# Performance work log

Measured on AMD Instinct MI355X. Metric: run time of the kernel, lower is better.

Reference implementation:

```python
import jax, jax.numpy as jnp
import numpy as np

B, N, E, H = 4, 2048, 1024, 16
Dh = E // H  # 64


def _rope_tables(n, dh, dtype=jnp.float32):
    inv_freq = 1.0 / (10000.0 ** (jnp.arange(0, dh, 2, dtype=jnp.float32) / dh))
    t = jnp.arange(n, dtype=jnp.float32)
    freqs = jnp.outer(t, inv_freq)            # (N, Dh/2)
    emb = jnp.concatenate([freqs, freqs], -1)  # (N, Dh)
    return jnp.cos(emb).astype(dtype), jnp.sin(emb).astype(dtype)


def _rotate_half(x):
    half = x.shape[-1] // 2
    return jnp.concatenate([-x[..., half:], x[..., :half]], axis=-1)


def _apply_rope(x, cos, sin):
    # x: (B, H, N, Dh); cos/sin: (N, Dh)
    return x * cos[None, None] + _rotate_half(x) * sin[None, None]


def setup_inputs() -> dict:
    key = jax.random.key(0)
    ks = jax.random.split(key, 10)
    x = jax.random.normal(ks[0], (B, N, E), dtype=jnp.float32)
    s = 0.02
    wq = jax.random.normal(ks[1], (E, E), jnp.float32) * s
    bq = jnp.zeros((E,), jnp.float32)
    wk = jax.random.normal(ks[2], (E, E), jnp.float32) * s
    bk = jnp.zeros((E,), jnp.float32)
    wv = jax.random.normal(ks[3], (E, E), jnp.float32) * s
    bv = jnp.zeros((E,), jnp.float32)
    wo = jax.random.normal(ks[4], (E, E), jnp.float32) * s
    bo = jnp.zeros((E,), jnp.float32)
    # no padding (all keys valid); flip some entries True to exercise masking if desired
    key_padding_mask = jnp.zeros((B, N), dtype=bool)
    return dict(x=x, wq=wq, bq=bq, wk=wk, bk=bk, wv=wv, bv=bv,
                wo=wo, bo=bo, key_padding_mask=key_padding_mask)


def reference(x, wq, bq, wk, bk, wv, bv, wo, bo, key_padding_mask):
    b, n, e = x.shape

    def proj(w, bvec):
        y = jnp.einsum('bne,fe->bnf', x, w) + bvec  # Linear: x @ W^T + b
        return y.reshape(b, n, H, Dh).transpose(0, 2, 1, 3)  # (B,H,N,Dh)

    Q, K, V = proj(wq, bq), proj(wk, bk), proj(wv, bv)
    cos, sin = _rope_tables(n, Dh, x.dtype)
    Q = _apply_rope(Q, cos, sin)
    K = _apply_rope(K, cos, sin)

    scale = Dh ** -0.5
    attn = jnp.einsum('bhqd,bhkd->bhqk', Q, K) * scale  # (B,H,N,N)
    attn = jnp.where(key_padding_mask[:, None, None, :], -jnp.inf, attn)
    attn = jax.nn.softmax(attn, axis=-1)
    out = jnp.einsum('bhqk,bhkd->bhqd', attn, V)
    out = out.transpose(0, 2, 1, 3).reshape(b, n, e)
    return jnp.einsum('bne,fe->bnf', out, wo) + bo
```

## Files before the change

### kernel.cpp

```cpp
#include <hip/hip_runtime.h>
#include <hip/hip_bf16.h>
#include <stdint.h>

#define B_   4
#define N_   2048
#define E_   1024
#define H_   16
#define DH_  64
#define M_   (B_*N_)
#define KD_  1024

typedef __bf16 bf16x8 __attribute__((ext_vector_type(8)));
typedef float  f32x4  __attribute__((ext_vector_type(4)));
typedef float  f32x16 __attribute__((ext_vector_type(16)));

__device__ __forceinline__ ushort f2bf(float f) {
  union { float f; uint32_t u; } x; x.f = f;
  uint32_t r = x.u + 0x7fffu + ((x.u >> 16) & 1u);
  return (ushort)(r >> 16);
}

__device__ __forceinline__ f32x4 mfma16(bf16x8 a, bf16x8 b, f32x4 c) {
  return __builtin_amdgcn_mfma_f32_16x16x32_bf16(a, b, c, 0, 0, 0);
}
__device__ __forceinline__ f32x16 mfma32(bf16x8 a, bf16x8 b, f32x16 c) {
  return __builtin_amdgcn_mfma_f32_32x32x16_bf16(a, b, c, 0, 0, 0);
}

__device__ __forceinline__ uint32_t cvtpk(float lo, float hi) {
  uint32_t d;
  asm("v_cvt_pk_bf16_f32 %0, %1, %2" : "=v"(d) : "v"(lo), "v"(hi));
  return d;
}

#if __has_builtin(__builtin_amdgcn_exp2f)
#define FEXP2(x) __builtin_amdgcn_exp2f(x)
#else
#define FEXP2(x) exp2f(x)
#endif

__device__ __forceinline__ void gload16(const void* g, void* l) {
  __builtin_amdgcn_global_load_lds(
      (const __attribute__((address_space(1))) uint32_t*)g,
      (__attribute__((address_space(3))) uint32_t*)l, 16, 0, 0);
}

__global__ void prep(const float* __restrict__ x,
                     const float* __restrict__ wq, const float* __restrict__ wk,
                     const float* __restrict__ wv, const float* __restrict__ wo,
                     ushort* __restrict__ xb, ushort* __restrict__ wqkv,
                     ushort* __restrict__ wob,
                     float* __restrict__ ct, float* __restrict__ st)
{
  int bid = blockIdx.x;
  if (bid < 8192) {
    int i = (bid * 256 + threadIdx.x) * 4;
    float4 v = *(const float4*)(x + i);
    ushort4 o; o.x = f2bf(v.x); o.y = f2bf(v.y); o.z = f2bf(v.z); o.w = f2bf(v.w);
    *(ushort4*)(xb + i) = o;
  } else if (bid < 12288) {
    int i = ((bid - 8192) * 256 + threadIdx.x) * 4;
    int which = i >> 20;
    int off = i & 1048575;
    const float* src = which == 0 ? wq : which == 1 ? wk : which == 2 ? wv : wo;
    float4 v = *(const float4*)(src + off);
    ushort4 o; o.x = f2bf(v.x); o.y = f2bf(v.y); o.z = f2bf(v.z); o.w = f2bf(v.w);
    if (which < 3) *(ushort4*)(wqkv + i) = o;
    else           *(ushort4*)(wob + off) = o;
  } else {
    int idx = (bid - 12288) * 256 + threadIdx.x;
    int n = idx >> 5, i = idx & 31;
    double inv = exp(-(double)i * (9.210340371976184 / 32.0));
    float ang = (float)n * (float)inv;
    ct[idx] = cosf(ang);
    st[idx] = sinf(ang);
  }
}

#define GEMM_KLOOP(Aptr, Wptr)                                                 \
  for (int k0 = 0; k0 < KD_; k0 += 64) {                                       \
    _Pragma("unroll")                                                          \
    for (int i = 0; i < 4; ++i) {                                              \
      uint32_t flat = i * 4096 + w * 1024 + lane * 16;                         \
      uint32_t row = flat >> 7, cb = flat & 127;                               \
      uint32_t cbs = cb ^ ((row & 7) << 4);                                    \
      gload16((const char*)(Aptr) + (size_t)(m0 + row) * 2048 + k0 * 2 + cbs,  \
              smA + i * 4096 + w * 1024);                                      \
      gload16((const char*)(Wptr) + (size_t)(n0 + row) * 2048 + k0 * 2 + cbs,  \
              smB + i * 4096 + w * 1024);                                      \
    }                                                                          \
    __syncthreads();                                                           \
    bf16x8 af[4][2], bfr[4][2];                                                \
    _Pragma("unroll")                                                          \
    for (int mf = 0; mf < 4; ++mf)                                             \
      _Pragma("unroll")                                                        \
      for (int kk = 0; kk < 2; ++kk) {                                         \
        int row = wr * 64 + mf * 16 + c;                                       \
        int cb = (kk * 64 + g * 16) ^ ((row & 7) << 4);                        \
        af[mf][kk] = *(const bf16x8*)(smA + row * 128 + cb);                   \
        int rowb = wc * 64 + mf * 16 + c;                                      \
        int cbb = (kk * 64 + g * 16) ^ ((rowb & 7) << 4);                      \
        bfr[mf][kk] = *(const bf16x8*)(smB + rowb * 128 + cbb);                \
      }                                                                        \
    _Pragma("unroll")                                                          \
    for (int kk = 0; kk < 2; ++kk)                                             \
      _Pragma("unroll")                                                        \
      for (int mf = 0; mf < 4; ++mf)                                           \
        _Pragma("unroll")                                                      \
        for (int nf = 0; nf < 4; ++nf)                                         \
          acc[mf][nf] = mfma16(af[mf][kk], bfr[nf][kk], acc[mf][nf]);          \
    __syncthreads();                                                           \
  }

__launch_bounds__(256, 3)
__global__ void gemm_qkv(const ushort* __restrict__ A, const ushort* __restrict__ W,
                         const float* __restrict__ bq, const float* __restrict__ bk,
                         const float* __restrict__ bv,
                         ushort* __restrict__ Qo, ushort* __restrict__ Ko,
                         ushort* __restrict__ Vto,
                         const float* __restrict__ cost, const float* __restrict__ sint)
{
  __shared__ char smem[32768];
  char* smA = smem;
  char* smB = smem + 16384;
  const int tid = threadIdx.x;
  const int lane = tid & 63, w = tid >> 6;
  const int c = lane & 15, g = lane >> 4;
  const int m0 = blockIdx.x * 128, n0 = blockIdx.y * 128;
  const int wr = w >> 1, wc = w & 1;

  f32x4 acc[4][4] = {};
  GEMM_KLOOP(A, W)

  const int sel = n0 >> 10;
  const int ncol = n0 & 1023;
  const int colbase = ncol + wc * 64;
  const int h = colbase >> 6;

  if (sel == 2) {
#pragma unroll
    for (int mf = 0; mf < 4; ++mf) {
      int tok = m0 + wr * 64 + mf * 16 + 4 * g;
      int b = tok >> 11, n = tok & 2047;
#pragma unroll
      for (int nf = 0; nf < 4; ++nf) {
        int d = nf * 16 + c;
        float bvv = bv[colbase + nf * 16 + c];
        ushort4 o;
        o.x = f2bf(acc[mf][nf][0] + bvv);
        o.y = f2bf(acc[mf][nf][1] + bvv);
        o.z = f2bf(acc[mf][nf][2] + bvv);
        o.w = f2bf(acc[mf][nf][3] + bvv);
        *(ushort4*)(Vto + (((size_t)(b * 16 + h) * 64 + d) << 11) + n) = o;
      }
    }
  } else {
    const float* bias = sel ? bk : bq;
    ushort* outB = sel ? Ko : Qo;
    const float sc = sel ? 1.0f : 0.125f * 1.44269504088896340736f;
#pragma unroll
    for (int mf = 0; mf < 4; ++mf) {
#pragma unroll
      for (int r = 0; r < 4; ++r) {
        int tok = m0 + wr * 64 + mf * 16 + 4 * g + r;
        int b = tok >> 11, n = tok & 2047;
        float v[4];
#pragma unroll
        for (int nf = 0; nf < 4; ++nf)
          v[nf] = acc[mf][nf][r] + bias[colbase + nf * 16 + c];
        ushort* orow = outB + ((size_t)(b * 16 + h) * 2048 + n) * 64;
#pragma unroll
        for (int nf = 0; nf < 2; ++nf) {
          int d = nf * 16 + c;
          float cv = cost[n * 32 + d];
          float sv = sint[n * 32 + d];
          orow[d]      = f2bf((v[nf] * cv - v[nf + 2] * sv) * sc);
          orow[d + 32] = f2bf((v[nf + 2] * cv + v[nf] * sv) * sc);
        }
      }
    }
  }
}

__launch_bounds__(256, 3)
__global__ void gemm_out(const ushort* __restrict__ A, const ushort* __restrict__ W,
                         const float* __restrict__ bias, float* __restrict__ outF)
{
  __shared__ char smem[32768];
  char* smA = smem;
  char* smB = smem + 16384;
  const int tid = threadIdx.x;
  const int lane = tid & 63, w = tid >> 6;
  const int c = lane & 15, g = lane >> 4;
  const int m0 = blockIdx.x * 128, n0 = blockIdx.y * 128;
  const int wr = w >> 1, wc = w & 1;

  f32x4 acc[4][4] = {};
  GEMM_KLOOP(A, W)

  const int colbase = n0 + wc * 64;
#pragma unroll
  for (int mf = 0; mf < 4; ++mf) {
    int rowb = m0 + wr * 64 + mf * 16 + 4 * g;
#pragma unroll
    for (int nf = 0; nf < 4; ++nf) {
      int f = colbase + nf * 16 + c;
      float bvv = bias[f];
#pragma unroll
      for (int r = 0; r < 4; ++r)
        outF[(size_t)(rowb + r) * 1024 + f] = acc[mf][nf][r] + bvv;
    }
  }
}

__launch_bounds__(512, 4)
__global__ void flash_k(const ushort* __restrict__ Q, const ushort* __restrict__ K,
                        const ushort* __restrict__ Vt, const uint8_t* __restrict__ mask,
                        ushort* __restrict__ O)
{
  __shared__ char smem[36864];
  const int tid = threadIdx.x;
  const int lane = tid & 63, w = tid >> 6;
  const int l31 = lane & 31, hi = lane >> 5;
  const int L = blockIdx.x;
  const int xcd = L & 7, slot = L >> 3;
  const int cc = slot >> 3, qb = slot & 7;
  const int b = cc >> 1, h = xcd + 8 * (cc & 1);
  const int q0 = qb * 256;
  const size_t head = (size_t)(b * 16 + h) * (2048 * 64);
  const ushort* Qh = Q + head;
  const uint8_t* mb = mask + b * 2048;

  const int qrow = q0 + w * 32 + l31;
  bf16x8 qf[4];
#pragma unroll
  for (int kk = 0; kk < 4; ++kk)
    qf[kk] = *(const bf16x8*)(Qh + (size_t)qrow * 64 + kk * 16 + hi * 8);

  uint64_t mm;
  {
    const uint64_t* m64 = (const uint64_t*)mb;
    mm = m64[lane * 4 + 0] | m64[lane * 4 + 1] | m64[lane * 4 + 2] | m64[lane * 4 + 3];
  }
  const bool anymask = __any(mm != 0);

  bf16x8 vones;
#pragma unroll
  for (int j = 0; j < 8; ++j) vones[j] = (__bf16)1.0f;

  f32x16 Oa0 = {}, Oa1 = {}, Sacc = {};

  const int srow = tid >> 3;
  const int scb = (tid & 7) * 16;
  const int cbs = scb ^ ((srow & 7) << 4);
  const char* Kg = (const char*)(K + head) + srow * 128 + cbs;
  const char* Vg = (const char*)(Vt + head) + srow * 4096 + cbs;

  gload16(Kg, smem + w * 1024);
  gload16(Vg, smem + 8192 + w * 1024);
  Kg += 8192;
  Vg += 128;
  __syncthreads();

  const int swz = (l31 & 7) << 4;

#define FLASH_TILE(T, CBUF, SBUF, DO_STAGE)                                    \
  {                                                                            \
    if (DO_STAGE) {                                                            \
      gload16(Kg, smem + (SBUF) + w * 1024);                                   \
      gload16(Vg, smem + (SBUF) + 8192 + w * 1024);                            \
      Kg += 8192; Vg += 128;                                                   \
    }                                                                          \
    const char* bK = smem + (CBUF);                                            \
    const char* bV = smem + (CBUF) + 8192;                                     \
    f32x16 s0 = {}, s1 = {};                                                   \
    __builtin_amdgcn_s_setprio(1);                                             \
    _Pragma("unroll")                                                          \
    for (int kk = 0; kk < 4; ++kk) {                                           \
      int col = (32 * kk + 16 * hi) ^ swz;                                     \
      bf16x8 k0 = *(const bf16x8*)(bK + l31 * 128 + col);                      \
      bf16x8 k1 = *(const bf16x8*)(bK + (l31 + 32) * 128 + col);               \
      s0 = mfma32(k0, qf[kk], s0);                                             \
      s1 = mfma32(k1, qf[kk], s1);                                             \
    }                                                                          \
    __builtin_amdgcn_s_setprio(0);                                             \
    float p0[16], p1[16];                                                      \
    _Pragma("unroll")                                                          \
    for (int i = 0; i < 16; ++i) {                                             \
      p0[i] = FEXP2(s0[i]);                                                    \
      p1[i] = FEXP2(s1[i]);                                                    \
    }                                                                          \
    if (anymask) {                                                             \
      int kv0 = (T) * 64;                                                      \
      _Pragma("unroll")                                                        \
      for (int r = 0; r < 16; ++r) {                                           \
        int crow = (r & 3) + 8 * (r >> 2) + 4 * hi;                            \
        if (mb[kv0 + crow]) p0[r] = 0.f;                                       \
        if (mb[kv0 + 32 + crow]) p1[r] = 0.f;                                  \
      }                                                                        \
    }                                                                          \
    uint32_t pw[4][4];                                                         \
    _Pragma("unroll")                                                          \
    for (int half = 0; half < 2; ++half) {                                     \
      const float* p = half ? p1 : p0;                                         \
      uint32_t alo0 = cvtpk(p[0], p[1]),  ahi0 = cvtpk(p[2], p[3]);            \
      uint32_t alo1 = cvtpk(p[4], p[5]),  ahi1 = cvtpk(p[6], p[7]);            \
      uint32_t alo2 = cvtpk(p[8], p[9]),  ahi2 = cvtpk(p[10], p[11]);          \
      uint32_t alo3 = cvtpk(p[12], p[13]), ahi3 = cvtpk(p[14], p[15]);         \
      auto r0 = __builtin_amdgcn_permlane32_swap(alo0, alo1, false, false);    \
      auto r1 = __builtin_amdgcn_permlane32_swap(ahi0, ahi1, false, false);    \
      auto r2 = __builtin_amdgcn_permlane32_swap(alo2, alo3, false, false);    \
      auto r3 = __builtin_amdgcn_permlane32_swap(ahi2, ahi3, false, false);    \
      pw[half * 2 + 0][0] = r0[0]; pw[half * 2 + 0][2] = r0[1];                \
      pw[half * 2 + 0][1] = r1[0]; pw[half * 2 + 0][3] = r1[1];                \
      pw[half * 2 + 1][0] = r2[0]; pw[half * 2 + 1][2] = r2[1];                \
      pw[half * 2 + 1][1] = r3[0]; pw[half * 2 + 1][3] = r3[1];                \
    }                                                                          \
    __builtin_amdgcn_s_setprio(1);                                             \
    _Pragma("unroll")                                                          \
    for (int c4 = 0; c4 < 4; ++c4) {                                           \
      union { uint32_t u[4]; bf16x8 v; } pf;                                   \
      pf.u[0] = pw[c4][0]; pf.u[1] = pw[c4][1];                                \
      pf.u[2] = pw[c4][2]; pf.u[3] = pw[c4][3];                                \
      int col = (32 * c4 + 16 * hi) ^ swz;                                     \
      bf16x8 v0 = *(const bf16x8*)(bV + l31 * 128 + col);                      \
      bf16x8 v1 = *(const bf16x8*)(bV + (l31 + 32) * 128 + col);               \
      Oa0 = mfma32(v0, pf.v, Oa0);                                             \
      Oa1 = mfma32(v1, pf.v, Oa1);                                             \
      Sacc = mfma32(vones, pf.v, Sacc);                                        \
    }                                                                          \
    __builtin_amdgcn_s_setprio(0);                                             \
    __syncthreads();                                                           \
  }

  for (int t = 0; t < N_ / 64; t += 2) {
    FLASH_TILE(t,     0,     16384, true)
    FLASH_TILE(t + 1, 16384, 0,     (t + 2 < N_ / 64))
  }
#undef FLASH_TILE

  float inv = 1.0f / Sacc[0];
  char* tr = smem + w * 4608;
#pragma unroll
  for (int db = 0; db < 2; ++db) {
    const f32x16& o = db ? Oa1 : Oa0;
#pragma unroll
    for (int a = 0; a < 4; ++a) {
      uint32_t lo = cvtpk(o[4 * a] * inv, o[4 * a + 1] * inv);
      uint32_t hi2 = cvtpk(o[4 * a + 2] * inv, o[4 * a + 3] * inv);
      *(uint2*)(tr + l31 * 144 + db * 64 + a * 16 + hi * 8) = make_uint2(lo, hi2);
    }
  }
  __asm__ volatile("" ::: "memory");
#pragma unroll
  for (int it = 0; it < 4; ++it) {
    uint4 v = *(const uint4*)(tr + l31 * 144 + it * 32 + hi * 16);
    int n = q0 + w * 32 + l31;
    *(uint4*)(O + (size_t)(b * 2048 + n) * 1024 + h * 64 + it * 16 + hi * 8) = v;
  }
}

extern "C" void kernel_launch(void* const* d_in, const int* in_sizes, int n_in,
                              void* d_out, int out_size, void* d_ws, size_t ws_size,
                              hipStream_t stream)
{
  (void)in_sizes; (void)n_in; (void)out_size; (void)ws_size;
  const float* x  = (const float*)d_in[0];
  const float* wq = (const float*)d_in[1];
  const float* bq = (const float*)d_in[2];
  const float* wk = (const float*)d_in[3];
  const float* bk = (const float*)d_in[4];
  const float* wv = (const float*)d_in[5];
  const float* bv = (const float*)d_in[6];
  const float* wo = (const float*)d_in[7];
  const float* bo = (const float*)d_in[8];
  const uint8_t* mask = (const uint8_t*)d_in[9];
  float* out = (float*)d_out;

  char* ws = (char*)d_ws;
  ushort* xb    = (ushort*)(ws + 0);
  ushort* Ab    = xb;
  ushort* wqkvb = (ushort*)(ws + 16777216);
  ushort* wob   = (ushort*)(ws + 23068672);
  ushort* Qb    = (ushort*)(ws + 25165824);
  ushort* Kb    = (ushort*)(ws + 41943040);
  ushort* Vtb   = (ushort*)(ws + 58720256);
  float*  cost  = (float*)(ws + 75497472);
  float*  sint  = (float*)(ws + 75759616);

  prep<<<12544, 256, 0, stream>>>(x, wq, wk, wv, wo, xb, wqkvb, wob, cost, sint);

  gemm_qkv<<<dim3(M_ / 128, 24), 256, 0, stream>>>(xb, wqkvb, bq, bk, bv,
                                                   Qb, Kb, Vtb, cost, sint);

  flash_k<<<512, 512, 0, stream>>>(Qb, Kb, Vtb, mask, Ab);

  gemm_out<<<dim3(M_ / 128, 8), 256, 0, stream>>>(Ab, wob, bo, out);
}
```

Before: 167.2 us.

## Rewrite QKV GEMM with 256x256 tiles, double-buffered LDS and XCD-aware block mapping

Replaces the 128x128 single-buffered QKV projection GEMM with a 512-thread kernel that computes 256x256 output tiles. It double-buffers the tiles in 128KB of LDS, interleaves the global loads for the next k-tile between sub-phases, and raises wave priority around the MFMA blocks. Block indices are remapped so that neighbouring M tiles land on the same XCD for L2 reuse, and the output GEMM gets the same XCD-aware mapping. The aim is more operand reuse and load latency hidden behind compute. The cost is one block per CU, higher register pressure, and 384 blocks that may not fill all 256 CUs evenly.

```diff
diff --git a/kernel.cpp b/kernel.cpp
--- a/kernel.cpp
+++ b/kernel.cpp
@@ -77,6 +77,152 @@
   }
 }
 
+__launch_bounds__(512, 1)
+__global__ void gemm_qkv8(const ushort* __restrict__ A, const ushort* __restrict__ W,
+                          const float* __restrict__ bq, const float* __restrict__ bk,
+                          const float* __restrict__ bv,
+                          ushort* __restrict__ Qo, ushort* __restrict__ Ko,
+                          ushort* __restrict__ Vto,
+                          const float* __restrict__ cost, const float* __restrict__ sint)
+{
+  __shared__ char smem[131072];
+  const int tid = threadIdx.x;
+  const int lane = tid & 63, w = tid >> 6;
+  const int c = lane & 15, g = lane >> 4;
+  const int wr = w & 3, wq = w >> 2;
+  const int bid = blockIdx.x;
+  const int mb = (bid & 7) * 4 + ((bid >> 3) & 3);
+  const int nb = bid >> 5;
+  const int m0 = mb * 256, n0 = nb * 256;
+
+  const int srow = tid >> 3;
+  const int scb = (tid & 7) * 16;
+  const int cbs = scb ^ ((srow & 7) << 4);
+  const char* gA0 = (const char*)A + (size_t)(m0 + srow) * 2048 + cbs;
+  const char* gB0 = (const char*)W + (size_t)(n0 + srow) * 2048 + cbs;
+
+  f32x4 acc[2][2][8] = {};
+
+#define STAGE_A8(KT, MH, DB)                                                   \
+  { const char* s_ = gA0 + (MH) * 262144 + (KT) * 128;                         \
+    gload16(s_,          smem + (DB) + (MH) * 16384 + w * 1024);               \
+    gload16(s_ + 131072, smem + (DB) + (MH) * 16384 + 8192 + w * 1024); }
+#define STAGE_B8(KT, HB, DB)                                                   \
+  { const char* s_ = gB0 + (HB) * 262144 + (KT) * 128;                         \
+    gload16(s_,          smem + (DB) + 32768 + (HB) * 16384 + w * 1024);       \
+    gload16(s_ + 131072, smem + (DB) + 32768 + (HB) * 16384 + 8192 + w * 1024); }
+
+#define PHASE8(MH, NH, DO_WAIT, STAGE_STMT)                                    \
+  {                                                                            \
+    if (DO_WAIT) asm volatile("s_waitcnt vmcnt(2)" ::: "memory");              \
+    __builtin_amdgcn_s_barrier();                                              \
+    const char* Ab = smem + cur + (MH) * 16384;                                \
+    const char* Bb = smem + cur + 32768 + wq * 16384;                          \
+    bf16x8 af[2][2], bfv[4][2];                                                \
+    _Pragma("unroll")                                                          \
+    for (int m = 0; m < 2; ++m)                                                \
+      _Pragma("unroll")                                                        \
+      for (int kk = 0; kk < 2; ++kk) {                                         \
+        int row = wr * 32 + m * 16 + c;                                        \
+        af[m][kk] = *(const bf16x8*)(Ab + row * 128 +                          \
+                                     ((kk * 64 + g * 16) ^ ((row & 7) << 4))); \
+      }                                                                        \
+    _Pragma("unroll")                                                          \
+    for (int j = 0; j < 4; ++j)                                                \
+      _Pragma("unroll")                                                        \
+      for (int kk = 0; kk < 2; ++kk) {                                         \
+        int row = (NH) * 64 + j * 16 + c;                                      \
+        bfv[j][kk] = *(const bf16x8*)(Bb + row * 128 +                         \
+                                      ((kk * 64 + g * 16) ^ ((row & 7) << 4)));\
+      }                                                                        \
+    STAGE_STMT;                                                                \
+    __builtin_amdgcn_s_setprio(1);                                             \
+    _Pragma("unroll")                                                          \
+    for (int kk = 0; kk < 2; ++kk)                                             \
+      _Pragma("unroll")                                                        \
+      for (int m = 0; m < 2; ++m)                                              \
+        _Pragma("unroll")                                                      \
+        for (int j = 0; j < 4; ++j)                                            \
+          acc[MH][m][(NH) * 4 + j] =                                           \
+              mfma16(af[m][kk], bfv[j][kk], acc[MH][m][(NH) * 4 + j]);         \
+    __builtin_amdgcn_s_setprio(0);                                             \
+  }
+
+  STAGE_B8(0, 0, 0)
+  STAGE_B8(0, 1, 0)
+  STAGE_A8(0, 0, 0)
+  STAGE_A8(0, 1, 0)
+
+  for (int t = 0; t < 16; ++t) {
+    const int cur = (t & 1) << 16;
+    const int nxt = cur ^ 65536;
+    const int kt = (t < 15) ? t + 1 : 15;
+    PHASE8(0, 0, true,  STAGE_B8(kt, 0, nxt))
+    PHASE8(1, 0, true,  STAGE_B8(kt, 1, nxt))
+    PHASE8(0, 1, false, STAGE_A8(kt, 0, nxt))
+    PHASE8(1, 1, false, STAGE_A8(kt, 1, nxt))
+  }
+#undef PHASE8
+#undef STAGE_A8
+#undef STAGE_B8
+
+  const int sel = n0 >> 10;
+  const int ncl = n0 & 1023;
+
+  if (sel == 2) {
+#pragma unroll
+    for (int mh = 0; mh < 2; ++mh)
+#pragma unroll
+      for (int m = 0; m < 2; ++m) {
+        int tok = m0 + mh * 128 + wr * 32 + m * 16 + 4 * g;
+        int b = tok >> 11, nn = tok & 2047;
+#pragma unroll
+        for (int n = 0; n < 8; ++n) {
+          int col = ncl + wq * 128 + n * 16 + c;
+          int h = col >> 6, d = col & 63;
+          float bvv = bv[col];
+          ushort4 o;
+          o.x = f2bf(acc[mh][m][n][0] + bvv);
+          o.y = f2bf(acc[mh][m][n][1] + bvv);
+          o.z = f2bf(acc[mh][m][n][2] + bvv);
+          o.w = f2bf(acc[mh][m][n][3] + bvv);
+          *(ushort4*)(Vto + (((size_t)(b * 16 + h) * 64 + d) << 11) + nn) = o;
+        }
+      }
+  } else {
+    const float* bias = sel ? bk : bq;
+    ushort* outB = sel ? Ko : Qo;
+    const float sc = sel ? 1.0f : 0.125f * 1.44269504088896340736f;
+#pragma unroll
+    for (int mh = 0; mh < 2; ++mh)
+#pragma unroll
+      for (int m = 0; m < 2; ++m)
+#pragma unroll
+        for (int r = 0; r < 4; ++r) {
+          int tok = m0 + mh * 128 + wr * 32 + m * 16 + 4 * g + r;
+          int b = tok >> 11, nn = tok & 2047;
+#pragma unroll
+          for (int hh = 0; hh < 2; ++hh) {
+            int hcol = ncl + wq * 128 + hh * 64;
+            int h = hcol >> 6;
+            float v[4];
+#pragma unroll
+            for (int j = 0; j < 4; ++j)
+              v[j] = acc[mh][m][hh * 4 + j][r] + bias[hcol + j * 16 + c];
+            ushort* orow = outB + ((size_t)(b * 16 + h) * 2048 + nn) * 64;
+#pragma unroll
+            for (int j = 0; j < 2; ++j) {
+              int d = j * 16 + c;
+              float cv = cost[nn * 32 + d];
+              float sv = sint[nn * 32 + d];
+              orow[d]      = f2bf((v[j] * cv - v[j + 2] * sv) * sc);
+              orow[d + 32] = f2bf((v[j + 2] * cv + v[j] * sv) * sc);
+            }
+          }
+        }
+  }
+}
+
 #define GEMM_KLOOP(Aptr, Wptr)                                                 \
   for (int k0 = 0; k0 < KD_; k0 += 64) {                                       \
     _Pragma("unroll")                                                          \
@@ -111,76 +257,6 @@
           acc[mf][nf] = mfma16(af[mf][kk], bfr[nf][kk], acc[mf][nf]);          \
     __syncthreads();                                                           \
   }
-
-__launch_bounds__(256, 3)
-__global__ void gemm_qkv(const ushort* __restrict__ A, const ushort* __restrict__ W,
-                         const float* __restrict__ bq, const float* __restrict__ bk,
-                         const float* __restrict__ bv,
-                         ushort* __restrict__ Qo, ushort* __restrict__ Ko,
-                         ushort* __restrict__ Vto,
-                         const float* __restrict__ cost, const float* __restrict__ sint)
-{
-  __shared__ char smem[32768];
-  char* smA = smem;
-  char* smB = smem + 16384;
-  const int tid = threadIdx.x;
-  const int lane = tid & 63, w = tid >> 6;
-  const int c = lane & 15, g = lane >> 4;
-  const int m0 = blockIdx.x * 128, n0 = blockIdx.y * 128;
-  const int wr = w >> 1, wc = w & 1;
-
-  f32x4 acc[4][4] = {};
-  GEMM_KLOOP(A, W)
-
-  const int sel = n0 >> 10;
-  const int ncol = n0 & 1023;
-  const int colbase = ncol + wc * 64;
-  const int h = colbase >> 6;
-
-  if (sel == 2) {
-#pragma unroll
-    for (int mf = 0; mf < 4; ++mf) {
-      int tok = m0 + wr * 64 + mf * 16 + 4 * g;
-      int b = tok >> 11, n = tok & 2047;
-#pragma unroll
-      for (int nf = 0; nf < 4; ++nf) {
-        int d = nf * 16 + c;
-        float bvv = bv[colbase + nf * 16 + c];
-        ushort4 o;
-        o.x = f2bf(acc[mf][nf][0] + bvv);
-        o.y = f2bf(acc[mf][nf][1] + bvv);
-        o.z = f2bf(acc[mf][nf][2] + bvv);
-        o.w = f2bf(acc[mf][nf][3] + bvv);
-        *(ushort4*)(Vto + (((size_t)(b * 16 + h) * 64 + d) << 11) + n) = o;
-      }
-    }
-  } else {
-    const float* bias = sel ? bk : bq;
-    ushort* outB = sel ? Ko : Qo;
-    const float sc = sel ? 1.0f : 0.125f * 1.44269504088896340736f;
-#pragma unroll
-    for (int mf = 0; mf < 4; ++mf) {
-#pragma unroll
-      for (int r = 0; r < 4; ++r) {
-        int tok = m0 + wr * 64 + mf * 16 + 4 * g + r;
-        int b = tok >> 11, n = tok & 2047;
-        float v[4];
-#pragma unroll
-        for (int nf = 0; nf < 4; ++nf)
-          v[nf] = acc[mf][nf][r] + bias[colbase + nf * 16 + c];
-        ushort* orow = outB + ((size_t)(b * 16 + h) * 2048 + n) * 64;
-#pragma unroll
-        for (int nf = 0; nf < 2; ++nf) {
-          int d = nf * 16 + c;
-          float cv = cost[n * 32 + d];
-          float sv = sint[n * 32 + d];
-          orow[d]      = f2bf((v[nf] * cv - v[nf + 2] * sv) * sc);
-          orow[d + 32] = f2bf((v[nf + 2] * cv + v[nf] * sv) * sc);
-        }
-      }
-    }
-  }
-}
 
 __launch_bounds__(256, 3)
 __global__ void gemm_out(const ushort* __restrict__ A, const ushort* __restrict__ W,
@@ -192,7 +268,10 @@
   const int tid = threadIdx.x;
   const int lane = tid & 63, w = tid >> 6;
   const int c = lane & 15, g = lane >> 4;
-  const int m0 = blockIdx.x * 128, n0 = blockIdx.y * 128;
+  const int bid = blockIdx.x;
+  const int xcd = bid & 7, j = bid >> 3;
+  const int m0 = (xcd * 8 + (j & 7)) * 128;
+  const int n0 = (j >> 3) * 128;
   const int wr = w >> 1, wc = w & 1;
 
   f32x4 acc[4][4] = {};
@@ -390,10 +469,10 @@
 
   prep<<<12544, 256, 0, stream>>>(x, wq, wk, wv, wo, xb, wqkvb, wob, cost, sint);
 
-  gemm_qkv<<<dim3(M_ / 128, 24), 256, 0, stream>>>(xb, wqkvb, bq, bk, bv,
-                                                   Qb, Kb, Vtb, cost, sint);
+  gemm_qkv8<<<384, 512, 0, stream>>>(xb, wqkvb, bq, bk, bv,
+                                     Qb, Kb, Vtb, cost, sint);
 
   flash_k<<<512, 512, 0, stream>>>(Qb, Kb, Vtb, mask, Ab);
 
-  gemm_out<<<dim3(M_ / 128, 8), 256, 0, stream>>>(Ab, wob, bo, out);
-}
+  gemm_out<<<512, 256, 0, stream>>>(Ab, wob, bo, out);
+}
```

After: 181.1 us. 1.08x slower.

## Replace QKV GEMM with 256x256-tile, 8-wave, double-buffered pipelined kernel

Applied to the files above, without the earlier changes.

Replaces the 128x128-tile QKV projection GEMM with a 256x256-tile kernel using 8 waves and 128KB of LDS. Global-to-LDS loads for the next K step are interleaved with MFMA work in four phases per iteration, with partial vmcnt waits and raw barriers. It also adds a block-index swizzle so blocks reuse data in L2, and raises MFMA priority with setprio. This trades occupancy (one block per CU) for more data reuse per tile and overlap of memory with compute, at the cost of fragile manual synchronisation and a grid of only 384 blocks.

```diff
diff --git a/kernel.cpp b/kernel.cpp
--- a/kernel.cpp
+++ b/kernel.cpp
@@ -77,6 +77,153 @@
   }
 }
 
+__launch_bounds__(512, 1)
+__global__ void gemm_qkv8(const ushort* __restrict__ A, const ushort* __restrict__ W,
+                          const float* __restrict__ bq, const float* __restrict__ bk,
+                          const float* __restrict__ bv,
+                          ushort* __restrict__ Qo, ushort* __restrict__ Ko,
+                          ushort* __restrict__ Vto,
+                          const float* __restrict__ cost, const float* __restrict__ sint)
+{
+  __shared__ char smem[131072];
+  const int tid = threadIdx.x;
+  const int lane = tid & 63, w = tid >> 6;
+  const int c = lane & 15, g = lane >> 4;
+  const int wn = w & 3, wm = w >> 2;
+  const int sbid = (blockIdx.x & 7) * 48 + (blockIdx.x >> 3);
+  const int m0 = (sbid / 12) * 256, n0 = (sbid % 12) * 256;
+
+  const int srow = tid >> 3;
+  const int scbs = ((tid & 7) * 16) ^ ((srow & 7) << 4);
+  const char* gA = (const char*)A + (size_t)(m0 + srow) * 2048 + scbs;
+  const char* gB = (const char*)W + (size_t)(n0 + srow) * 2048 + scbs;
+
+  f32x4 acc[8][4] = {};
+
+#define STGA(HH, TT, DB) {                                                     \
+    const char* s_ = gA + (size_t)(HH) * 262144 + (TT) * 128;                  \
+    gload16(s_,          smem + (DB) + (HH) * 16384 + tid * 16);               \
+    gload16(s_ + 131072, smem + (DB) + (HH) * 16384 + 8192 + tid * 16); }
+#define STGB(HH, TT, DB) {                                                     \
+    const char* s_ = gB + (size_t)(HH) * 262144 + (TT) * 128;                  \
+    gload16(s_,          smem + (DB) + 32768 + (HH) * 16384 + tid * 16);       \
+    gload16(s_ + 131072, smem + (DB) + 32768 + (HH) * 16384 + 8192 + tid * 16); }
+
+#define RD_B()                                                                 \
+    _Pragma("unroll") for (int n = 0; n < 4; ++n)                              \
+    _Pragma("unroll") for (int kk = 0; kk < 2; ++kk) {                         \
+      int row = wn * 64 + n * 16 + c;                                          \
+      bfr[n][kk] = *(const bf16x8*)(smem + cur + 32768 + row * 128 +           \
+                                    ((kk * 64 + g * 16) ^ ((row & 7) << 4)));  \
+    }
+#define RD_A(Q)                                                                \
+    bf16x8 af[2][2];                                                           \
+    _Pragma("unroll") for (int m = 0; m < 2; ++m)                              \
+    _Pragma("unroll") for (int kk = 0; kk < 2; ++kk) {                         \
+      int row = wm * 128 + (Q) * 32 + m * 16 + c;                              \
+      af[m][kk] = *(const bf16x8*)(smem + cur + row * 128 +                    \
+                                   ((kk * 64 + g * 16) ^ ((row & 7) << 4)));   \
+    }
+#define MM(Q)                                                                  \
+    __builtin_amdgcn_s_setprio(1);                                             \
+    _Pragma("unroll") for (int kk = 0; kk < 2; ++kk)                           \
+    _Pragma("unroll") for (int m = 0; m < 2; ++m)                              \
+    _Pragma("unroll") for (int n = 0; n < 4; ++n)                              \
+      acc[(Q) * 2 + m][n] = mfma16(af[m][kk], bfr[n][kk], acc[(Q) * 2 + m][n]);\
+    __builtin_amdgcn_s_setprio(0);
+
+  STGA(0, 0, 0) STGA(1, 0, 0) STGB(0, 0, 0) STGB(1, 0, 0)
+  STGB(0, 1, 65536) STGB(1, 1, 65536)
+
+  bf16x8 bfr[4][2];
+  for (int T = 0; T < 16; ++T) {
+    const int cur = (T & 1) << 16, oth = cur ^ 65536;
+    asm volatile("s_waitcnt vmcnt(4)" ::: "memory");
+    __builtin_amdgcn_s_barrier();
+    asm volatile("" ::: "memory");
+    {
+      RD_B(); RD_A(0)
+      STGA(0, T + 1, oth)
+      MM(0)
+    }
+    __builtin_amdgcn_s_barrier();
+    asm volatile("" ::: "memory");
+    {
+      RD_A(1)
+      STGA(1, T + 1, oth)
+      MM(1)
+    }
+    __builtin_amdgcn_s_barrier();
+    asm volatile("" ::: "memory");
+    {
+      RD_A(2)
+      STGB(0, T + 2, cur)
+      MM(2)
+    }
+    __builtin_amdgcn_s_barrier();
+    asm volatile("" ::: "memory");
+    {
+      RD_A(3)
+      STGB(1, T + 2, cur)
+      MM(3)
+    }
+  }
+#undef STGA
+#undef STGB
+#undef RD_B
+#undef RD_A
+#undef MM
+
+  const int sel = n0 >> 10;
+  const int ncl = n0 & 1023;
+  const int hcol = ncl + wn * 64;
+  const int h = hcol >> 6;
+
+  if (sel == 2) {
+#pragma unroll
+    for (int mf = 0; mf < 8; ++mf) {
+      int tok = m0 + wm * 128 + mf * 16 + 4 * g;
+      int b = tok >> 11, nn = tok & 2047;
+#pragma unroll
+      for (int n = 0; n < 4; ++n) {
+        int d = n * 16 + c;
+        float bvv = bv[hcol + d];
+        ushort4 o;
+        o.x = f2bf(acc[mf][n][0] + bvv);
+        o.y = f2bf(acc[mf][n][1] + bvv);
+        o.z = f2bf(acc[mf][n][2] + bvv);
+        o.w = f2bf(acc[mf][n][3] + bvv);
+        *(ushort4*)(Vto + (((size_t)(b * 16 + h) * 64 + d) << 11) + nn) = o;
+      }
+    }
+  } else {
+    const float* bias = sel ? bk : bq;
+    ushort* outB = sel ? Ko : Qo;
+    const float sc = sel ? 1.0f : 0.125f * 1.44269504088896340736f;
+#pragma unroll
+    for (int mf = 0; mf < 8; ++mf) {
+#pragma unroll
+      for (int r = 0; r < 4; ++r) {
+        int tok = m0 + wm * 128 + mf * 16 + 4 * g + r;
+        int b = tok >> 11, nn = tok & 2047;
+        float v[4];
+#pragma unroll
+        for (int n = 0; n < 4; ++n)
+          v[n] = acc[mf][n][r] + bias[hcol + n * 16 + c];
+        ushort* orow = outB + ((size_t)(b * 16 + h) * 2048 + nn) * 64;
+#pragma unroll
+        for (int nf = 0; nf < 2; ++nf) {
+          int d = nf * 16 + c;
+          float cv = cost[nn * 32 + d];
+          float sv = sint[nn * 32 + d];
+          orow[d]      = f2bf((v[nf] * cv - v[nf + 2] * sv) * sc);
+          orow[d + 32] = f2bf((v[nf + 2] * cv + v[nf] * sv) * sc);
+        }
+      }
+    }
+  }
+}
+
 #define GEMM_KLOOP(Aptr, Wptr)                                                 \
   for (int k0 = 0; k0 < KD_; k0 += 64) {                                       \
     _Pragma("unroll")                                                          \
@@ -111,76 +258,6 @@
           acc[mf][nf] = mfma16(af[mf][kk], bfr[nf][kk], acc[mf][nf]);          \
     __syncthreads();                                                           \
   }
-
-__launch_bounds__(256, 3)
-__global__ void gemm_qkv(const ushort* __restrict__ A, const ushort* __restrict__ W,
-                         const float* __restrict__ bq, const float* __restrict__ bk,
-                         const float* __restrict__ bv,
-                         ushort* __restrict__ Qo, ushort* __restrict__ Ko,
-                         ushort* __restrict__ Vto,
-                         const float* __restrict__ cost, const float* __restrict__ sint)
-{
-  __shared__ char smem[32768];
-  char* smA = smem;
-  char* smB = smem + 16384;
-  const int tid = threadIdx.x;
-  const int lane = tid & 63, w = tid >> 6;
-  const int c = lane & 15, g = lane >> 4;
-  const int m0 = blockIdx.x * 128, n0 = blockIdx.y * 128;
-  const int wr = w >> 1, wc = w & 1;
-
-  f32x4 acc[4][4] = {};
-  GEMM_KLOOP(A, W)
-
-  const int sel = n0 >> 10;
-  const int ncol = n0 & 1023;
-  const int colbase = ncol + wc * 64;
-  const int h = colbase >> 6;
-
-  if (sel == 2) {
-#pragma unroll
-    for (int mf = 0; mf < 4; ++mf) {
-      int tok = m0 + wr * 64 + mf * 16 + 4 * g;
-      int b = tok >> 11, n = tok & 2047;
-#pragma unroll
-      for (int nf = 0; nf < 4; ++nf) {
-        int d = nf * 16 + c;
-        float bvv = bv[colbase + nf * 16 + c];
-        ushort4 o;
-        o.x = f2bf(acc[mf][nf][0] + bvv);
-        o.y = f2bf(acc[mf][nf][1] + bvv);
-        o.z = f2bf(acc[mf][nf][2] + bvv);
-        o.w = f2bf(acc[mf][nf][3] + bvv);
-        *(ushort4*)(Vto + (((size_t)(b * 16 + h) * 64 + d) << 11) + n) = o;
-      }
-    }
-  } else {
-    const float* bias = sel ? bk : bq;
-    ushort* outB = sel ? Ko : Qo;
-    const float sc = sel ? 1.0f : 0.125f * 1.44269504088896340736f;
-#pragma unroll
-    for (int mf = 0; mf < 4; ++mf) {
-#pragma unroll
-      for (int r = 0; r < 4; ++r) {
-        int tok = m0 + wr * 64 + mf * 16 + 4 * g + r;
-        int b = tok >> 11, n = tok & 2047;
-        float v[4];
-#pragma unroll
-        for (int nf = 0; nf < 4; ++nf)
-          v[nf] = acc[mf][nf][r] + bias[colbase + nf * 16 + c];
-        ushort* orow = outB + ((size_t)(b * 16 + h) * 2048 + n) * 64;
-#pragma unroll
-        for (int nf = 0; nf < 2; ++nf) {
-          int d = nf * 16 + c;
-          float cv = cost[n * 32 + d];
-          float sv = sint[n * 32 + d];
-          orow[d]      = f2bf((v[nf] * cv - v[nf + 2] * sv) * sc);
-          orow[d + 32] = f2bf((v[nf + 2] * cv + v[nf] * sv) * sc);
-        }
-      }
-    }
-  }
-}
 
 __launch_bounds__(256, 3)
 __global__ void gemm_out(const ushort* __restrict__ A, const ushort* __restrict__ W,
@@ -390,8 +467,8 @@
 
   prep<<<12544, 256, 0, stream>>>(x, wq, wk, wv, wo, xb, wqkvb, wob, cost, sint);
 
-  gemm_qkv<<<dim3(M_ / 128, 24), 256, 0, stream>>>(xb, wqkvb, bq, bk, bv,
-                                                   Qb, Kb, Vtb, cost, sint);
+  gemm_qkv8<<<384, 512, 0, stream>>>(xb, wqkvb, bq, bk, bv,
+                                     Qb, Kb, Vtb, cost, sint);
 
   flash_k<<<512, 512, 0, stream>>>(Qb, Kb, Vtb, mask, Ab);
 
```

Result: slower. 178.2 us (+6.6%).
